# Kernel tuning notes

Hardware: AMD Instinct MI355X
Metric: run time of the kernel (lower is better)

## Reference

```python
import jax, jax.numpy as jnp
import numpy as np

T_PAD, C_PAD = 8, 8   # padded LUT dims (Liberty LUTs are <=8x8 here)
EPS = 1e-12


def _sorted_table(key, n, m):
    # strictly increasing per-row breakpoint tables
    steps = jax.random.uniform(key, (n, m), minval=0.01, maxval=1.0, dtype=jnp.float32)
    return jnp.cumsum(steps, axis=1)


def _interp_all(x_t, x_c, vals, t_tbl, c_tbl, td, cd):
    """Vectorized LUT lookup: scalar / 1D-trans / 1D-cap / 2D bilinear, masked.
    x_t,x_c: [B]; vals: [B, T*C]; t_tbl: [B,T]; c_tbl: [B,C]; td,cd: [B] int.
    """
    B = x_t.shape[0]
    rows = jnp.arange(B)
    ss = jax.vmap(lambda tbl, x: jnp.searchsorted(tbl, x, side='right'))
    max_t = jnp.maximum(td - 1, 0)
    max_c = jnp.maximum(cd - 1, 0)
    # clamp(min=1) then clamp(max=actual-1), matching torch sequential clamps
    t_hi = jnp.minimum(jnp.maximum(ss(t_tbl, x_t), 1), max_t)
    c_hi = jnp.minimum(jnp.maximum(ss(c_tbl, x_c), 1), max_c)
    t_lo = jnp.maximum(t_hi - 1, 0)
    c_lo = jnp.maximum(c_hi - 1, 0)
    t0 = t_tbl[rows, t_lo]; t1 = t_tbl[rows, t_hi]
    c0 = c_tbl[rows, c_lo]; c1 = c_tbl[rows, c_hi]
    ti = t1 - t0; ci = c1 - c0
    t_deg = jnp.abs(ti) < EPS
    c_deg = jnp.abs(ci) < EPS
    xt = jnp.clip(x_t, t0, t1)
    xc = jnp.clip(x_c, c0, c1)
    ti_s = jnp.where(t_deg, EPS, ti)
    ci_s = jnp.where(c_deg, EPS, ci)
    ft = jnp.clip((xt - t0) / ti_s, 0.0, 1.0)
    fc = jnp.clip((xc - c0) / ci_s, 0.0, 1.0)
    # ---- 2D bilinear (row-major with ACTUAL cap-dim stride, as in torch code)
    v00 = vals[rows, t_lo * cd + c_lo]
    v01 = vals[rows, t_lo * cd + c_hi]
    v10 = vals[rows, t_hi * cd + c_lo]
    v11 = vals[rows, t_hi * cd + c_hi]
    wa = (t1 - xt) * (c1 - xc)
    wb = (t1 - xt) * (xc - c0)
    wc_ = (xt - t0) * (c1 - xc)
    wd = (xt - t0) * (xc - c0)
    bil = (v00 * wa + v01 * wb + v10 * wc_ + v11 * wd) / (ti_s * ci_s)
    val2d = jnp.where(t_deg & c_deg, v00,
            jnp.where(t_deg, v00 + (v01 - v00) * fc,
            jnp.where(c_deg, v00 + (v10 - v00) * ft, bil)))
    # ---- 1D over trans (cap dim <= 1 -> values row is effectively [T])
    y0t = vals[rows, t_lo]; y1t = vals[rows, t_hi]
    val1t = jnp.where(t_deg, y0t, y0t + (y1t - y0t) * ft)
    # ---- 1D over cap (trans dim <= 1 -> values row is effectively [C])
    y0c = vals[rows, c_lo]; y1c = vals[rows, c_hi]
    val1c = jnp.where(c_deg, y0c, y0c + (y1c - y0c) * fc)
    # ---- scalar
    val_s = vals[rows, 0]
    is2d = (td > 1) & (cd > 1)
    is1t = (td > 1) & (cd <= 1)
    is1c = (td <= 1) & (cd > 1)
    valid = (td > 0) & (cd > 0)
    out = jnp.where(is2d, val2d,
          jnp.where(is1t, val1t,
          jnp.where(is1c, val1c, val_s)))
    return jnp.where(valid, out, jnp.zeros_like(out))


def setup_inputs() -> dict:
    N_ARCS, B = 500_000, 2_000_000
    k = jax.random.key(0)
    k1, k2, k3, k4, k5, k6, k7 = jax.random.split(k, 7)
    trans_tbl = _sorted_table(k1, N_ARCS, T_PAD)        # [N, 8] sorted
    cap_tbl = _sorted_table(k2, N_ARCS, C_PAD)          # [N, 8] sorted
    values = jax.random.normal(k3, (N_ARCS, T_PAD * C_PAD), dtype=jnp.float32)
    dims = jax.random.randint(k4, (N_ARCS, 2), 0, T_PAD + 1, dtype=jnp.int32)
    arc_idxs = jax.random.randint(k5, (B,), 0, N_ARCS, dtype=jnp.int32)
    input_trans = jax.random.uniform(k6, (B,), minval=0.0, maxval=9.0, dtype=jnp.float32)
    output_caps = jax.random.uniform(k7, (B,), minval=0.0, maxval=9.0, dtype=jnp.float32)
    return {
        'input_trans': input_trans,
        'output_caps': output_caps,
        'arc_idxs': arc_idxs,
        'flat_luts_values': values,
        'flat_luts_trans_table': trans_tbl,
        'flat_luts_cap_table': cap_tbl,
        'flat_luts_dim': dims,
    }


def reference(input_trans, output_caps, arc_idxs, flat_luts_values,
              flat_luts_trans_table, flat_luts_cap_table, flat_luts_dim):
    # per-eval gather of LUT rows (the irregular-access hot spot)
    vals = flat_luts_values[arc_idxs]          # [B, 64]
    t_tbl = flat_luts_trans_table[arc_idxs]    # [B, 8]
    c_tbl = flat_luts_cap_table[arc_idxs]      # [B, 8]
    td = flat_luts_dim[arc_idxs, 0]
    cd = flat_luts_dim[arc_idxs, 1]
    return _interp_all(input_trans, output_caps, vals, t_tbl, c_tbl, td, cd)
```

## Files before the change

### kernel.cpp

```cpp
#include <hip/hip_runtime.h>

#define EPS 1e-12f

typedef float vf4 __attribute__((ext_vector_type(4)));
typedef int   vi2 __attribute__((ext_vector_type(2)));

__device__ __forceinline__ float sel8(const vf4& a, const vf4& b, int i) {
    float lo = (i == 0) ? a.x : (i == 1) ? a.y : (i == 2) ? a.z : a.w;
    float hi = (i == 4) ? b.x : (i == 5) ? b.y : (i == 6) ? b.z : b.w;
    return (i < 4) ? lo : hi;
}

__device__ __forceinline__ float sel4(const vf4& q, int i) {
    return (i == 0) ? q.x : (i == 1) ? q.y : (i == 2) ? q.z : q.w;
}

__global__ __launch_bounds__(256) void k_repack(const float* __restrict__ t_table,
                                                const float* __restrict__ c_table,
                                                const int* __restrict__ dims,
                                                vf4* __restrict__ packed,
                                                unsigned char* __restrict__ dims8,
                                                int N) {
    int a = blockIdx.x * blockDim.x + threadIdx.x;
    if (a >= N) return;
    const vf4* tt = (const vf4*)(t_table + (size_t)a * 8);
    const vf4* cc = (const vf4*)(c_table + (size_t)a * 8);
    vf4 t0 = __builtin_nontemporal_load(tt);
    vf4 t1 = __builtin_nontemporal_load(tt + 1);
    vf4 c0 = __builtin_nontemporal_load(cc);
    vf4 c1 = __builtin_nontemporal_load(cc + 1);
    vf4* dst = packed + (size_t)a * 4;
    dst[0] = t0;
    dst[1] = t1;
    dst[2] = c0;
    dst[3] = c1;
    vi2 d = __builtin_nontemporal_load((const vi2*)dims + a);
    dims8[a] = (unsigned char)((d.x & 0xF) | ((d.y & 0xF) << 4));
}

__global__ __launch_bounds__(256) void k_main_d8(
    const float* __restrict__ x_t_arr, const float* __restrict__ x_c_arr,
    const int* __restrict__ arcs, const float* __restrict__ values,
    const vf4* __restrict__ packed, const unsigned char* __restrict__ dims8,
    float* __restrict__ out, int B)
{
    int i = blockIdx.x * blockDim.x + threadIdx.x;
    if (i >= B) return;
    float x_t = __builtin_nontemporal_load(x_t_arr + i);
    float x_c = __builtin_nontemporal_load(x_c_arr + i);
    int arc = __builtin_nontemporal_load(arcs + i);

    unsigned char dp = dims8[arc];
    int td = dp & 0xF, cd = dp >> 4;
    if (td == 0 || cd == 0) { __builtin_nontemporal_store(0.0f, out + i); return; }

    const vf4* rec = packed + (size_t)arc * 4;
    vf4 ta = rec[0], tb = rec[1], ca = rec[2], cb = rec[3];

    int ss_t = (ta.x <= x_t) + (ta.y <= x_t) + (ta.z <= x_t) + (ta.w <= x_t)
             + (tb.x <= x_t) + (tb.y <= x_t) + (tb.z <= x_t) + (tb.w <= x_t);
    int ss_c = (ca.x <= x_c) + (ca.y <= x_c) + (ca.z <= x_c) + (ca.w <= x_c)
             + (cb.x <= x_c) + (cb.y <= x_c) + (cb.z <= x_c) + (cb.w <= x_c);

    int t_hi = min(max(ss_t, 1), max(td - 1, 0));
    int c_hi = min(max(ss_c, 1), max(cd - 1, 0));
    int t_lo = max(t_hi - 1, 0);
    int c_lo = max(c_hi - 1, 0);

    float t0 = sel8(ta, tb, t_lo), t1 = sel8(ta, tb, t_hi);
    float c0 = sel8(ca, cb, c_lo), c1 = sel8(ca, cb, c_hi);

    float ti = t1 - t0, ci = c1 - c0;
    float xt = fminf(fmaxf(x_t, t0), t1);
    float xc = fminf(fmaxf(x_c, c0), c1);
    float ti_s = (fabsf(ti) < EPS) ? EPS : ti;
    float ci_s = (fabsf(ci) < EPS) ? EPS : ci;
    float ft = fminf(fmaxf((xt - t0) / ti_s, 0.f), 1.f);
    float fc = fminf(fmaxf((xc - c0) / ci_s, 0.f), 1.f);

    bool is2d = (td > 1) && (cd > 1);
    bool is1t = (td > 1) && (cd <= 1);
    bool is1c = (td <= 1) && (cd > 1);

    int iA = is2d ? (t_lo * cd + c_lo) : is1t ? t_lo : is1c ? c_lo : 0;
    int iB = is2d ? (t_hi * cd + c_lo) : is1t ? t_hi : iA;
    int dA = (is2d || is1c) ? 1 : 0;
    int dB = is2d ? 1 : 0;

    const float* vrow = values + (size_t)arc * 64;
    int bA = iA & ~3, oA = iA & 3;
    int bB = iB & ~3, oB = iB & 3;
    vf4 qA = *(const vf4*)(vrow + bA);
    vf4 qB = *(const vf4*)(vrow + bB);
    float v00 = sel4(qA, oA);
    float v10 = sel4(qB, oB);
    float v01 = (oA + dA <= 3) ? sel4(qA, oA + dA) : vrow[iA + dA];
    float v11 = (oB + dB <= 3) ? sel4(qB, oB + dB) : vrow[iB + dB];

    float wa = (t1 - xt) * (c1 - xc);
    float wb = (t1 - xt) * (xc - c0);
    float wc = (xt - t0) * (c1 - xc);
    float wd = (xt - t0) * (xc - c0);
    float bil = (v00 * wa + v01 * wb + v10 * wc + v11 * wd) / (ti_s * ci_s);

    float lin_t = v00 + (v10 - v00) * ft;
    float lin_c = v00 + (v01 - v00) * fc;

    float r = is2d ? bil : is1t ? lin_t : is1c ? lin_c : v00;
    __builtin_nontemporal_store(r, out + i);
}

__global__ __launch_bounds__(256) void TimingPropagation_35622458753425_kernel(
    const float* __restrict__ x_t_arr, const float* __restrict__ x_c_arr,
    const int* __restrict__ arcs, const float* __restrict__ values,
    const float* __restrict__ t_table, const float* __restrict__ c_table,
    const int* __restrict__ dims, float* __restrict__ out, int B)
{
    int i = blockIdx.x * blockDim.x + threadIdx.x;
    if (i >= B) return;
    int arc = arcs[i];
    int td = dims[2 * arc], cd = dims[2 * arc + 1];
    if (td == 0 || cd == 0) { out[i] = 0.0f; return; }
    float x_t = x_t_arr[i], x_c = x_c_arr[i];
    const vf4* tt = (const vf4*)(t_table + (size_t)arc * 8);
    const vf4* cc = (const vf4*)(c_table + (size_t)arc * 8);
    vf4 ta = tt[0], tb = tt[1], ca = cc[0], cb = cc[1];
    int ss_t = (ta.x <= x_t) + (ta.y <= x_t) + (ta.z <= x_t) + (ta.w <= x_t)
             + (tb.x <= x_t) + (tb.y <= x_t) + (tb.z <= x_t) + (tb.w <= x_t);
    int ss_c = (ca.x <= x_c) + (ca.y <= x_c) + (ca.z <= x_c) + (ca.w <= x_c)
             + (cb.x <= x_c) + (cb.y <= x_c) + (cb.z <= x_c) + (cb.w <= x_c);
    int t_hi = min(max(ss_t, 1), max(td - 1, 0));
    int c_hi = min(max(ss_c, 1), max(cd - 1, 0));
    int t_lo = max(t_hi - 1, 0);
    int c_lo = max(c_hi - 1, 0);
    float t0 = sel8(ta, tb, t_lo), t1 = sel8(ta, tb, t_hi);
    float c0 = sel8(ca, cb, c_lo), c1 = sel8(ca, cb, c_hi);
    float ti = t1 - t0, ci = c1 - c0;
    float xt = fminf(fmaxf(x_t, t0), t1);
    float xc = fminf(fmaxf(x_c, c0), c1);
    float ti_s = (fabsf(ti) < EPS) ? EPS : ti;
    float ci_s = (fabsf(ci) < EPS) ? EPS : ci;
    float ft = fminf(fmaxf((xt - t0) / ti_s, 0.f), 1.f);
    float fc = fminf(fmaxf((xc - c0) / ci_s, 0.f), 1.f);
    bool is2d = (td > 1) && (cd > 1);
    bool is1t = (td > 1) && (cd <= 1);
    bool is1c = (td <= 1) && (cd > 1);
    int i00 = is2d ? (t_lo * cd + c_lo) : is1t ? t_lo : is1c ? c_lo : 0;
    int i01 = is2d ? (t_lo * cd + c_hi) : is1c ? c_hi : i00;
    int i10 = is2d ? (t_hi * cd + c_lo) : is1t ? t_hi : i00;
    int i11 = is2d ? (t_hi * cd + c_hi) : i00;
    const float* vrow = values + (size_t)arc * 64;
    float v00 = vrow[i00], v01 = vrow[i01], v10 = vrow[i10], v11 = vrow[i11];
    float wa = (t1 - xt) * (c1 - xc);
    float wb = (t1 - xt) * (xc - c0);
    float wc = (xt - t0) * (c1 - xc);
    float wd = (xt - t0) * (xc - c0);
    float bil = (v00 * wa + v01 * wb + v10 * wc + v11 * wd) / (ti_s * ci_s);
    float lin_t = v00 + (v10 - v00) * ft;
    float lin_c = v00 + (v01 - v00) * fc;
    out[i] = is2d ? bil : is1t ? lin_t : is1c ? lin_c : v00;
}

extern "C" void kernel_launch(void* const* d_in, const int* in_sizes, int n_in,
                              void* d_out, int out_size, void* d_ws, size_t ws_size,
                              hipStream_t stream) {
    const float* x_t   = (const float*)d_in[0];
    const float* x_c   = (const float*)d_in[1];
    const int*   arcs  = (const int*)d_in[2];
    const float* vals  = (const float*)d_in[3];
    const float* t_tbl = (const float*)d_in[4];
    const float* c_tbl = (const float*)d_in[5];
    const int*   dims  = (const int*)d_in[6];
    float* out = (float*)d_out;
    int B = in_sizes[0];
    int N = in_sizes[3] / 64;

    size_t need_tc = (size_t)N * 64;
    size_t need_d8 = need_tc + (size_t)N;

    int gridB = (B + 255) / 256;
    int gridN = (N + 255) / 256;

    if (ws_size >= need_d8) {
        vf4* packed = (vf4*)d_ws;
        unsigned char* dims8 = (unsigned char*)d_ws + need_tc;
        k_repack<<<gridN, 256, 0, stream>>>(t_tbl, c_tbl, dims, packed, dims8, N);
        k_main_d8<<<gridB, 256, 0, stream>>>(x_t, x_c, arcs, vals, packed, dims8, out, B);
    } else {
        TimingPropagation_35622458753425_kernel<<<gridB, 256, 0, stream>>>(
            x_t, x_c, arcs, vals, t_tbl, c_tbl, dims, out, B);
    }
}
```

Before: 270.8 us.

## Drop repack pre-pass and read LUT tables directly in a single kernel

Removes the per-call repack kernel that copied trans/cap tables into a packed workspace record and compressed dims to bytes. The main kernel now loads the original tables with vector loads and reads dims as an int2, issuing those loads before the early-exit check. This saves one kernel launch and a full pass over the per-arc tables. In exchange each lookup touches three separate arrays instead of one packed record plus a byte array, which may lower cache locality for the random gathers.

```diff
diff --git a/kernel.cpp b/kernel.cpp
--- a/kernel.cpp
+++ b/kernel.cpp
@@ -15,34 +15,11 @@
     return (i == 0) ? q.x : (i == 1) ? q.y : (i == 2) ? q.z : q.w;
 }
 
-__global__ __launch_bounds__(256) void k_repack(const float* __restrict__ t_table,
-                                                const float* __restrict__ c_table,
-                                                const int* __restrict__ dims,
-                                                vf4* __restrict__ packed,
-                                                unsigned char* __restrict__ dims8,
-                                                int N) {
-    int a = blockIdx.x * blockDim.x + threadIdx.x;
-    if (a >= N) return;
-    const vf4* tt = (const vf4*)(t_table + (size_t)a * 8);
-    const vf4* cc = (const vf4*)(c_table + (size_t)a * 8);
-    vf4 t0 = __builtin_nontemporal_load(tt);
-    vf4 t1 = __builtin_nontemporal_load(tt + 1);
-    vf4 c0 = __builtin_nontemporal_load(cc);
-    vf4 c1 = __builtin_nontemporal_load(cc + 1);
-    vf4* dst = packed + (size_t)a * 4;
-    dst[0] = t0;
-    dst[1] = t1;
-    dst[2] = c0;
-    dst[3] = c1;
-    vi2 d = __builtin_nontemporal_load((const vi2*)dims + a);
-    dims8[a] = (unsigned char)((d.x & 0xF) | ((d.y & 0xF) << 4));
-}
-
-__global__ __launch_bounds__(256) void k_main_d8(
+__global__ __launch_bounds__(256) void TimingPropagation_35622458753425_kernel(
     const float* __restrict__ x_t_arr, const float* __restrict__ x_c_arr,
     const int* __restrict__ arcs, const float* __restrict__ values,
-    const vf4* __restrict__ packed, const unsigned char* __restrict__ dims8,
-    float* __restrict__ out, int B)
+    const float* __restrict__ t_table, const float* __restrict__ c_table,
+    const int* __restrict__ dims, float* __restrict__ out, int B)
 {
     int i = blockIdx.x * blockDim.x + threadIdx.x;
     if (i >= B) return;
@@ -50,12 +27,16 @@
     float x_c = __builtin_nontemporal_load(x_c_arr + i);
     int arc = __builtin_nontemporal_load(arcs + i);
 
-    unsigned char dp = dims8[arc];
-    int td = dp & 0xF, cd = dp >> 4;
+    vi2 d = *(const vi2*)(dims + (size_t)2 * arc);
+    const vf4* tt = (const vf4*)(t_table + (size_t)arc * 8);
+    const vf4* cc = (const vf4*)(c_table + (size_t)arc * 8);
+    vf4 ta = tt[0];
+    vf4 tb = tt[1];
+    vf4 ca = cc[0];
+    vf4 cb = cc[1];
+
+    int td = d.x, cd = d.y;
     if (td == 0 || cd == 0) { __builtin_nontemporal_store(0.0f, out + i); return; }
-
-    const vf4* rec = packed + (size_t)arc * 4;
-    vf4 ta = rec[0], tb = rec[1], ca = rec[2], cb = rec[3];
 
     int ss_t = (ta.x <= x_t) + (ta.y <= x_t) + (ta.z <= x_t) + (ta.w <= x_t)
              + (tb.x <= x_t) + (tb.y <= x_t) + (tb.z <= x_t) + (tb.w <= x_t);
@@ -110,57 +91,6 @@
     __builtin_nontemporal_store(r, out + i);
 }
 
-__global__ __launch_bounds__(256) void TimingPropagation_35622458753425_kernel(
-    const float* __restrict__ x_t_arr, const float* __restrict__ x_c_arr,
-    const int* __restrict__ arcs, const float* __restrict__ values,
-    const float* __restrict__ t_table, const float* __restrict__ c_table,
-    const int* __restrict__ dims, float* __restrict__ out, int B)
-{
-    int i = blockIdx.x * blockDim.x + threadIdx.x;
-    if (i >= B) return;
-    int arc = arcs[i];
-    int td = dims[2 * arc], cd = dims[2 * arc + 1];
-    if (td == 0 || cd == 0) { out[i] = 0.0f; return; }
-    float x_t = x_t_arr[i], x_c = x_c_arr[i];
-    const vf4* tt = (const vf4*)(t_table + (size_t)arc * 8);
-    const vf4* cc = (const vf4*)(c_table + (size_t)arc * 8);
-    vf4 ta = tt[0], tb = tt[1], ca = cc[0], cb = cc[1];
-    int ss_t = (ta.x <= x_t) + (ta.y <= x_t) + (ta.z <= x_t) + (ta.w <= x_t)
-             + (tb.x <= x_t) + (tb.y <= x_t) + (tb.z <= x_t) + (tb.w <= x_t);
-    int ss_c = (ca.x <= x_c) + (ca.y <= x_c) + (ca.z <= x_c) + (ca.w <= x_c)
-             + (cb.x <= x_c) + (cb.y <= x_c) + (cb.z <= x_c) + (cb.w <= x_c);
-    int t_hi = min(max(ss_t, 1), max(td - 1, 0));
-    int c_hi = min(max(ss_c, 1), max(cd - 1, 0));
-    int t_lo = max(t_hi - 1, 0);
-    int c_lo = max(c_hi - 1, 0);
-    float t0 = sel8(ta, tb, t_lo), t1 = sel8(ta, tb, t_hi);
-    float c0 = sel8(ca, cb, c_lo), c1 = sel8(ca, cb, c_hi);
-    float ti = t1 - t0, ci = c1 - c0;
-    float xt = fminf(fmaxf(x_t, t0), t1);
-    float xc = fminf(fmaxf(x_c, c0), c1);
-    float ti_s = (fabsf(ti) < EPS) ? EPS : ti;
-    float ci_s = (fabsf(ci) < EPS) ? EPS : ci;
-    float ft = fminf(fmaxf((xt - t0) / ti_s, 0.f), 1.f);
-    float fc = fminf(fmaxf((xc - c0) / ci_s, 0.f), 1.f);
-    bool is2d = (td > 1) && (cd > 1);
-    bool is1t = (td > 1) && (cd <= 1);
-    bool is1c = (td <= 1) && (cd > 1);
-    int i00 = is2d ? (t_lo * cd + c_lo) : is1t ? t_lo : is1c ? c_lo : 0;
-    int i01 = is2d ? (t_lo * cd + c_hi) : is1c ? c_hi : i00;
-    int i10 = is2d ? (t_hi * cd + c_lo) : is1t ? t_hi : i00;
-    int i11 = is2d ? (t_hi * cd + c_hi) : i00;
-    const float* vrow = values + (size_t)arc * 64;
-    float v00 = vrow[i00], v01 = vrow[i01], v10 = vrow[i10], v11 = vrow[i11];
-    float wa = (t1 - xt) * (c1 - xc);
-    float wb = (t1 - xt) * (xc - c0);
-    float wc = (xt - t0) * (c1 - xc);
-    float wd = (xt - t0) * (xc - c0);
-    float bil = (v00 * wa + v01 * wb + v10 * wc + v11 * wd) / (ti_s * ci_s);
-    float lin_t = v00 + (v10 - v00) * ft;
-    float lin_c = v00 + (v01 - v00) * fc;
-    out[i] = is2d ? bil : is1t ? lin_t : is1c ? lin_c : v00;
-}
-
 extern "C" void kernel_launch(void* const* d_in, const int* in_sizes, int n_in,
                               void* d_out, int out_size, void* d_ws, size_t ws_size,
                               hipStream_t stream) {
@@ -173,21 +103,10 @@
     const int*   dims  = (const int*)d_in[6];
     float* out = (float*)d_out;
     int B = in_sizes[0];
-    int N = in_sizes[3] / 64;
 
-    size_t need_tc = (size_t)N * 64;
-    size_t need_d8 = need_tc + (size_t)N;
+    (void)d_ws; (void)ws_size;
 
     int gridB = (B + 255) / 256;
-    int gridN = (N + 255) / 256;
-
-    if (ws_size >= need_d8) {
-        vf4* packed = (vf4*)d_ws;
-        unsigned char* dims8 = (unsigned char*)d_ws + need_tc;
-        k_repack<<<gridN, 256, 0, stream>>>(t_tbl, c_tbl, dims, packed, dims8, N);
-        k_main_d8<<<gridB, 256, 0, stream>>>(x_t, x_c, arcs, vals, packed, dims8, out, B);
-    } else {
-        TimingPropagation_35622458753425_kernel<<<gridB, 256, 0, stream>>>(
-            x_t, x_c, arcs, vals, t_tbl, c_tbl, dims, out, B);
-    }
+    TimingPropagation_35622458753425_kernel<<<gridB, 256, 0, stream>>>(
+        x_t, x_c, arcs, vals, t_tbl, c_tbl, dims, out, B);
 }
```

New measurement: 291.8 us. 1.08x slower.
